# Kernel tuning notes

Hardware: AMD Instinct MI355X
Metric: run time of the kernel (lower is better)

The kernel has to match this reference:

```python
import jax, jax.numpy as jnp
import numpy as np
import math

B, L, H, NH = 8, 512, 512, 8
DH = H // NH


def setup_inputs() -> dict:
    key = jax.random.key(0)
    ks = jax.random.split(key, 12)
    src = jax.random.normal(ks[0], (B, L, H), dtype=jnp.float32)
    seq_len = jax.random.randint(ks[1], (B,), L // 2, L + 1).astype(jnp.int32)
    seq_len = seq_len.at[0].set(L)  # guarantee max(seq_len) == L
    pe = jax.random.normal(ks[2], (2 * L, H), dtype=jnp.float32) * 0.02
    s = 1.0 / math.sqrt(H)
    Wq = jax.random.normal(ks[3], (H, H), dtype=jnp.float32) * s
    bq = jnp.zeros((H,), jnp.float32)
    Wk = jax.random.normal(ks[4], (H, H), dtype=jnp.float32) * s
    bk = jnp.zeros((H,), jnp.float32)
    Wv = jax.random.normal(ks[5], (H, H), dtype=jnp.float32) * s
    bv = jnp.zeros((H,), jnp.float32)
    Wr = jax.random.normal(ks[6], (H, H), dtype=jnp.float32) * s
    br = jnp.zeros((H,), jnp.float32)
    u = jax.random.normal(ks[7], (NH, DH), dtype=jnp.float32) * 0.02
    v = jax.random.normal(ks[8], (NH, DH), dtype=jnp.float32) * 0.02
    gamma = jnp.ones((H,), jnp.float32)
    beta = jnp.zeros((H,), jnp.float32)
    return dict(src=src, seq_len=seq_len, pe=pe, Wq=Wq, bq=bq, Wk=Wk, bk=bk,
                Wv=Wv, bv=bv, Wr=Wr, br=br, u=u, v=v, gamma=gamma, beta=beta)


def reference(src, seq_len, pe, Wq, bq, Wk, bk, Wv, bv, Wr, br, u, v, gamma, beta):
    b, l, h = src.shape
    dh = h // NH
    # relative distance rel[i,j] = j - i, lookup pe[rel + L]  -> [L, L, H]
    rel = jnp.arange(l)[None, :] - jnp.arange(l)[:, None]
    R = pe[rel + l]
    # projections (torch Linear: y = x W^T + b)
    q = src @ Wq.T + bq
    k = src @ Wk.T + bk
    val = src @ Wv.T + bv
    R = R @ Wr.T + br
    # split heads
    q = q.reshape(b, l, NH, dh)
    k = k.reshape(b, l, NH, dh)
    val = val.reshape(b, l, NH, dh)
    R = R.reshape(l, l, NH, dh)
    # Transformer-XL score terms
    A = jnp.einsum('bihd,bjhd->bhij', q, k)
    Bt = jnp.einsum('bihd,ijhd->bhij', q, R)
    C = jnp.einsum('hd,bjhd->bhj', u, k)[:, :, None, :]
    D = jnp.einsum('ijhd,hd->hij', R, v)[None]
    scores = (A + Bt + C + D) / math.sqrt(dh)
    # key-side padding mask
    mask = jnp.arange(l)[None, :] < seq_len[:, None]  # [B, L]
    scores = jnp.where(mask[:, None, None, :], scores, jnp.float32(-1e15))
    attn = jax.nn.softmax(scores, axis=-1)
    out = jnp.einsum('bhij,bjhd->bihd', attn, val).reshape(b, l, h)
    res = src + out
    # LayerNorm (eps=1e-5) then exact GELU
    mu = jnp.mean(res, axis=-1, keepdims=True)
    var = jnp.mean((res - mu) ** 2, axis=-1, keepdims=True)
    ln = (res - mu) * jax.lax.rsqrt(var + 1e-5) * gamma + beta
    return jax.nn.gelu(ln, approximate=False)
```

## Files before the change

### kernel.cpp

```cpp
#include <hip/hip_runtime.h>
#include <math.h>

#define Bn 8
#define Ln 512
#define Hn 512
#define NHn 8
#define DHn 64

typedef __attribute__((ext_vector_type(8))) short short8;
typedef __attribute__((ext_vector_type(4))) float f32x4;

__device__ __forceinline__ unsigned short f2bf(float f) {
    unsigned int u = __float_as_uint(f);
    unsigned int r = (u + 0x7FFFu + ((u >> 16) & 1u)) >> 16;
    return (unsigned short)r;
}
__device__ __forceinline__ float bf2f(unsigned short s) {
    return __uint_as_float(((unsigned int)s) << 16);
}

__device__ __forceinline__ void gload_lds16(const void* g, void* l) {
    __builtin_amdgcn_global_load_lds(
        (const __attribute__((address_space(1))) unsigned int*)g,
        (__attribute__((address_space(3))) unsigned int*)l,
        16, 0, 0);
}

__global__ __launch_bounds__(256) void convert_kernel(
    const float* __restrict__ src, const float* __restrict__ pe,
    const float* __restrict__ Wq, const float* __restrict__ Wk,
    const float* __restrict__ Wv, const float* __restrict__ Wr,
    const float* __restrict__ bq, const float* __restrict__ bk,
    const float* __restrict__ bv,
    unsigned short* __restrict__ src_bf, unsigned short* __restrict__ pe_bf,
    unsigned short* __restrict__ Wcat_bf, unsigned short* __restrict__ Wr_bf,
    float* __restrict__ bcat)
{
    const int bid = blockIdx.x;
    const int tid = threadIdx.x;
    const float* in; unsigned short* outp; int base4;
    if (bid < 2048)      { in = src; outp = src_bf;           base4 = bid; }
    else if (bid < 2560) { in = pe;  outp = pe_bf;            base4 = bid - 2048; }
    else if (bid < 2816) { in = Wq;  outp = Wcat_bf;          base4 = bid - 2560; }
    else if (bid < 3072) { in = Wk;  outp = Wcat_bf + 262144; base4 = bid - 2816; }
    else if (bid < 3328) { in = Wv;  outp = Wcat_bf + 524288; base4 = bid - 3072; }
    else if (bid < 3584) { in = Wr;  outp = Wr_bf;            base4 = bid - 3328; }
    else {
        const int idx = (bid - 3584) * 256 + tid;
        if (idx < 512)            bcat[idx] = bq[idx];
        else if (idx < 1024)      bcat[idx] = bk[idx - 512];
        else if (idx < 1536)      bcat[idx] = bv[idx - 1024];
        return;
    }
    const int i4 = (base4 * 256 + tid) * 4;
    float4 x = *(const float4*)&in[i4];
    ushort4 o;
    o.x = f2bf(x.x); o.y = f2bf(x.y); o.z = f2bf(x.z); o.w = f2bf(x.w);
    *(ushort4*)&outp[i4] = o;
}

__global__ __launch_bounds__(256) void mfma_nt_kernel(
    const unsigned short* __restrict__ src_bf,
    const unsigned short* __restrict__ Wcat_bf,
    const float* __restrict__ bcat,
    unsigned short* __restrict__ QKb,
    unsigned short* __restrict__ VTg,
    const unsigned short* __restrict__ pe_bf,
    const unsigned short* __restrict__ Wr_bf,
    const float* __restrict__ br,
    unsigned short* __restrict__ Rpb)
{
    const unsigned short* A; const unsigned short* B;
    int m0, n0, mode;
    if (blockIdx.z == 0) {
        if (blockIdx.x < 8) {
            mode = 0; A = src_bf;  m0 = blockIdx.y * 128;
            B = Wcat_bf; n0 = blockIdx.x * 128;
        } else {
            mode = 1; A = Wcat_bf; m0 = blockIdx.x * 128;
            B = src_bf;  n0 = blockIdx.y * 128;
        }
    } else {
        if (blockIdx.x >= 4 || blockIdx.y >= 8) return;
        mode = 2; A = pe_bf; m0 = blockIdx.y * 128;
        B = Wr_bf; n0 = blockIdx.x * 128;
    }

    __shared__ unsigned short As[128 * 32];
    __shared__ unsigned short Bs[128 * 32];

    const int t = threadIdx.x;
    const int wave = t >> 6, lane = t & 63;
    const int wm = (wave >> 1) * 64;
    const int wn = (wave & 1) * 64;

    f32x4 acc[4][4] = {};

    const int srow = wave * 32 + (lane >> 2);
    const int scol = (lane & 3) * 8;
    const unsigned short* Ag = A + (size_t)(m0 + srow) * 512 + scol;
    const unsigned short* Bg = B + (size_t)(n0 + srow) * 512 + scol;
    unsigned short* AsW = &As[srow * 32 + scol];
    unsigned short* BsW = &Bs[srow * 32 + scol];

    for (int k0 = 0; k0 < 512; k0 += 32) {
        __syncthreads();
        gload_lds16(Ag + k0,            AsW);
        gload_lds16(Ag + k0 + 16 * 512, AsW + 16 * 32);
        gload_lds16(Bg + k0,            BsW);
        gload_lds16(Bg + k0 + 16 * 512, BsW + 16 * 32);
        __syncthreads();

        short8 af[4], bf[4];
        #pragma unroll
        for (int mt = 0; mt < 4; ++mt)
            af[mt] = *(const short8*)&As[(wm + mt * 16 + (lane & 15)) * 32 + (lane >> 4) * 8];
        #pragma unroll
        for (int nt = 0; nt < 4; ++nt)
            bf[nt] = *(const short8*)&Bs[(wn + nt * 16 + (lane & 15)) * 32 + (lane >> 4) * 8];
        #pragma unroll
        for (int mt = 0; mt < 4; ++mt)
            #pragma unroll
            for (int nt = 0; nt < 4; ++nt)
                acc[mt][nt] = __builtin_amdgcn_mfma_f32_16x16x32_bf16(
                    af[mt], bf[nt], acc[mt][nt], 0, 0, 0);
    }

    const int crow = (lane >> 4) * 4;
    const int ccol = lane & 15;
    if (mode == 0) {
        #pragma unroll
        for (int mt = 0; mt < 4; ++mt)
            #pragma unroll
            for (int nt = 0; nt < 4; ++nt) {
                const int n = n0 + wn + nt * 16 + ccol;
                const float bn = bcat[n];
                #pragma unroll
                for (int r = 0; r < 4; ++r) {
                    const int m = m0 + wm + mt * 16 + crow + r;
                    QKb[(size_t)m * 1024 + n] = f2bf(acc[mt][nt][r] + bn);
                }
            }
    } else if (mode == 1) {
        #pragma unroll
        for (int mt = 0; mt < 4; ++mt)
            #pragma unroll
            for (int nt = 0; nt < 4; ++nt) {
                const int n = n0 + wn + nt * 16 + ccol;
                #pragma unroll
                for (int r = 0; r < 4; ++r) {
                    const int m = m0 + wm + mt * 16 + crow + r;
                    VTg[(size_t)(m - 1024) * 4096 + n] = f2bf(acc[mt][nt][r] + bcat[m]);
                }
            }
    } else {
        #pragma unroll
        for (int mt = 0; mt < 4; ++mt)
            #pragma unroll
            for (int nt = 0; nt < 4; ++nt) {
                const int n = n0 + wn + nt * 16 + ccol;
                const float bn = br[n];
                #pragma unroll
                for (int r = 0; r < 4; ++r) {
                    const int m = m0 + wm + mt * 16 + crow + r;
                    Rpb[(size_t)m * 512 + n] = f2bf(acc[mt][nt][r] + bn);
                }
            }
    }
}

#define PADK 72
#define QRS 133
__global__ __launch_bounds__(256) void attn_kernel(
    const unsigned short* __restrict__ QKb,
    const unsigned short* __restrict__ VTg,
    const unsigned short* __restrict__ Rpb,
    const float* __restrict__ u, const float* __restrict__ v,
    const int* __restrict__ seq_len, float* __restrict__ O)
{
    const int i0 = blockIdx.x * 64;
    const int h  = blockIdx.y;
    const int b  = blockIdx.z;
    const int slen = seq_len[b];

    __shared__ unsigned short k_s [64 * PADK];
    __shared__ unsigned short vT_s[64 * PADK];
    __shared__ unsigned short rs_s[64 * PADK];
    __shared__ unsigned short p_s [64 * PADK];
    __shared__ unsigned short qrT [64 * QRS];

    const int t = threadIdx.x;
    const int wave = t >> 6, lane = t & 63;
    const int l = lane & 15, g = lane >> 4;

    short8 af_qu[2], af_qv[2];
    {
        const unsigned short* qrow =
            QKb + (size_t)(b * 512 + i0 + wave * 16 + l) * 1024 + h * 64;
        #pragma unroll
        for (int kk = 0; kk < 2; ++kk) {
            const int c = kk * 32 + g * 8;
            unsigned short q8[8];
            *(uint4*)q8 = *(const uint4*)(qrow + c);
            float4 u0 = *(const float4*)(u + h * 64 + c);
            float4 u1 = *(const float4*)(u + h * 64 + c + 4);
            float4 v0 = *(const float4*)(v + h * 64 + c);
            float4 v1 = *(const float4*)(v + h * 64 + c + 4);
            float uf[8] = {u0.x,u0.y,u0.z,u0.w,u1.x,u1.y,u1.z,u1.w};
            float vf[8] = {v0.x,v0.y,v0.z,v0.w,v1.x,v1.y,v1.z,v1.w};
            short8 qu, qv;
            #pragma unroll
            for (int e = 0; e < 8; ++e) {
                float qf = bf2f(q8[e]);
                qu[e] = (short)f2bf(qf + uf[e]);
                qv[e] = (short)f2bf(qf + vf[e]);
            }
            af_qu[kk] = qu; af_qv[kk] = qv;
        }
    }

    float m_run[4], l_run[4];
    f32x4 accO[4] = {};
    #pragma unroll
    for (int r = 0; r < 4; ++r) { m_run[r] = -3.0e38f; l_run[r] = 0.f; }

    const int jr = t >> 2, c0 = (t & 3) * 16;

    for (int jt = 0; jt < 8; ++jt) {
        const int j0 = jt * 64;
        __syncthreads();

        {
            const unsigned short* kp =
                QKb + (size_t)(b * 512 + j0 + jr) * 1024 + 512 + h * 64 + c0;
            *(uint4*)(k_s + jr * PADK + c0)     = *(const uint4*)(kp);
            *(uint4*)(k_s + jr * PADK + c0 + 8) = *(const uint4*)(kp + 8);
            const unsigned short* vp =
                VTg + (size_t)(h * 64 + jr) * 4096 + b * 512 + j0 + c0;
            *(uint4*)(vT_s + jr * PADK + c0)     = *(const uint4*)(vp);
            *(uint4*)(vT_s + jr * PADK + c0 + 8) = *(const uint4*)(vp + 8);
        }

        const int nchunk = (jt == 0) ? 2 : 1;
        for (int c = 0; c < nchunk; ++c) {
            const int g_base = (jt == 0) ? (448 - i0 + 64 * c) : (j0 - i0 + 512);
            {
                const unsigned short* rp =
                    Rpb + (size_t)(g_base + jr) * 512 + h * 64 + c0;
                *(uint4*)(rs_s + jr * PADK + c0)     = *(const uint4*)(rp);
                *(uint4*)(rs_s + jr * PADK + c0 + 8) = *(const uint4*)(rp + 8);
            }
            __syncthreads();
            const int slot0 = (g_base & 127);
            #pragma unroll
            for (int nt8 = 0; nt8 < 4; ++nt8) {
                f32x4 a = {};
                #pragma unroll
                for (int kk = 0; kk < 2; ++kk) {
                    short8 br8 = *(const short8*)&rs_s[(nt8 * 16 + l) * PADK + kk * 32 + g * 8];
                    a = __builtin_amdgcn_mfma_f32_16x16x32_bf16(af_qv[kk], br8, a, 0, 0, 0);
                }
                const int sl = slot0 + nt8 * 16 + l;
                #pragma unroll
                for (int r = 0; r < 4; ++r)
                    qrT[(wave * 16 + g * 4 + r) * QRS + sl] = f2bf(a[r]);
            }
            if (c + 1 < nchunk) __syncthreads();
        }
        __syncthreads();

        f32x4 accA[4];
        #pragma unroll
        for (int nt = 0; nt < 4; ++nt) {
            f32x4 a = {};
            #pragma unroll
            for (int kk = 0; kk < 2; ++kk) {
                short8 bk = *(const short8*)&k_s[(nt * 16 + l) * PADK + kk * 32 + g * 8];
                a = __builtin_amdgcn_mfma_f32_16x16x32_bf16(af_qu[kk], bk, a, 0, 0, 0);
            }
            accA[nt] = a;
        }

        float sv[4][4];
        #pragma unroll
        for (int nt = 0; nt < 4; ++nt)
            #pragma unroll
            for (int r = 0; r < 4; ++r) {
                const int il = wave * 16 + g * 4 + r;
                const int slot = (j0 + nt * 16 + l - i0 - il + 512) & 127;
                const float qr = bf2f(qrT[il * QRS + slot]);
                float s = (accA[nt][r] + qr) * 0.125f;
                if (j0 + nt * 16 + l >= slen) s = -1e15f;
                sv[nt][r] = s;
            }

        float alpha_r[4];
        #pragma unroll
        for (int r = 0; r < 4; ++r) {
            float tm = fmaxf(fmaxf(sv[0][r], sv[1][r]), fmaxf(sv[2][r], sv[3][r]));
            tm = fmaxf(tm, __shfl_xor(tm, 1, 64));
            tm = fmaxf(tm, __shfl_xor(tm, 2, 64));
            tm = fmaxf(tm, __shfl_xor(tm, 4, 64));
            tm = fmaxf(tm, __shfl_xor(tm, 8, 64));
            const float mn = fmaxf(m_run[r], tm);
            alpha_r[r] = __expf(m_run[r] - mn);
            m_run[r] = mn;
            float ss = 0.f;
            #pragma unroll
            for (int nt = 0; nt < 4; ++nt) {
                const float p = __expf(sv[nt][r] - mn);
                sv[nt][r] = p; ss += p;
            }
            ss += __shfl_xor(ss, 1, 64);
            ss += __shfl_xor(ss, 2, 64);
            ss += __shfl_xor(ss, 4, 64);
            ss += __shfl_xor(ss, 8, 64);
            l_run[r] = l_run[r] * alpha_r[r] + ss;
        }

        #pragma unroll
        for (int nt = 0; nt < 4; ++nt)
            #pragma unroll
            for (int r = 0; r < 4; ++r)
                p_s[(wave * 16 + g * 4 + r) * PADK + nt * 16 + l] = f2bf(sv[nt][r]);
        __builtin_amdgcn_sched_barrier(0);

        #pragma unroll
        for (int nt = 0; nt < 4; ++nt)
            #pragma unroll
            for (int r = 0; r < 4; ++r)
                accO[nt][r] *= alpha_r[r];

        short8 pa[2];
        #pragma unroll
        for (int kk = 0; kk < 2; ++kk)
            pa[kk] = *(const short8*)&p_s[(wave * 16 + l) * PADK + kk * 32 + g * 8];
        #pragma unroll
        for (int nt = 0; nt < 4; ++nt) {
            #pragma unroll
            for (int kk = 0; kk < 2; ++kk) {
                short8 bv8 = *(const short8*)&vT_s[(nt * 16 + l) * PADK + kk * 32 + g * 8];
                accO[nt] = __builtin_amdgcn_mfma_f32_16x16x32_bf16(pa[kk], bv8, accO[nt], 0, 0, 0);
            }
        }
    }

    float inv[4];
    #pragma unroll
    for (int r = 0; r < 4; ++r) inv[r] = 1.0f / l_run[r];
    #pragma unroll
    for (int nt = 0; nt < 4; ++nt)
        #pragma unroll
        for (int r = 0; r < 4; ++r)
            O[(size_t)(b * 512 + i0 + wave * 16 + g * 4 + r) * 512 + h * 64 + nt * 16 + l]
                = accO[nt][r] * inv[r];
}

__global__ __launch_bounds__(256) void ln_gelu_kernel(
    const float* __restrict__ src, const float* __restrict__ O,
    const float* __restrict__ gamma, const float* __restrict__ beta,
    float* __restrict__ out)
{
    const int row  = blockIdx.x * 4 + (threadIdx.x >> 6);
    const int lane = threadIdx.x & 63;
    const float* s = &src[(size_t)row * 512];
    const float* o = &O[(size_t)row * 512];
    float x[8];
    float sum = 0.f;
    #pragma unroll
    for (int e = 0; e < 8; ++e) {
        x[e] = s[lane + e * 64] + o[lane + e * 64];
        sum += x[e];
    }
    #pragma unroll
    for (int off = 32; off >= 1; off >>= 1) sum += __shfl_xor(sum, off, 64);
    const float mean = sum * (1.0f / 512.0f);
    float var = 0.f;
    #pragma unroll
    for (int e = 0; e < 8; ++e) { float d = x[e] - mean; var += d * d; }
    #pragma unroll
    for (int off = 32; off >= 1; off >>= 1) var += __shfl_xor(var, off, 64);
    var *= (1.0f / 512.0f);
    const float inv = rsqrtf(var + 1e-5f);
    #pragma unroll
    for (int e = 0; e < 8; ++e) {
        const int c = lane + e * 64;
        float ln = (x[e] - mean) * inv * gamma[c] + beta[c];
        out[(size_t)row * 512 + c] = 0.5f * ln * (1.0f + erff(ln * 0.70710678118654752f));
    }
}

extern "C" void kernel_launch(void* const* d_in, const int* in_sizes, int n_in,
                              void* d_out, int out_size, void* d_ws, size_t ws_size,
                              hipStream_t stream)
{
    const float* src     = (const float*)d_in[0];
    const int*   seq_len = (const int*)  d_in[1];
    const float* pe      = (const float*)d_in[2];
    const float* Wq      = (const float*)d_in[3];
    const float* bq      = (const float*)d_in[4];
    const float* Wk      = (const float*)d_in[5];
    const float* bk      = (const float*)d_in[6];
    const float* Wv      = (const float*)d_in[7];
    const float* bv      = (const float*)d_in[8];
    const float* Wr      = (const float*)d_in[9];
    const float* br      = (const float*)d_in[10];
    const float* u       = (const float*)d_in[11];
    const float* v       = (const float*)d_in[12];
    const float* gamma   = (const float*)d_in[13];
    const float* beta    = (const float*)d_in[14];
    float* out = (float*)d_out;

    char* w = (char*)d_ws;
    unsigned short* QKb     = (unsigned short*)(w);
    unsigned short* VTg     = (unsigned short*)(w + 8388608);
    unsigned short* Rpb     = (unsigned short*)(w + 12582912);
    float*          O       = (float*)         (w + 13631488);
    unsigned short* src_bf  = (unsigned short*)(w + 22020096);
    unsigned short* pe_bf   = (unsigned short*)(w + 26214400);
    unsigned short* Wcat_bf = (unsigned short*)(w + 27262976);
    unsigned short* Wr_bf   = (unsigned short*)(w + 28835840);
    float*          bcat    = (float*)         (w + 29360128);

    convert_kernel<<<dim3(3590), 256, 0, stream>>>(
        src, pe, Wq, Wk, Wv, Wr, bq, bk, bv,
        src_bf, pe_bf, Wcat_bf, Wr_bf, bcat);

    mfma_nt_kernel<<<dim3(12, 32, 2), 256, 0, stream>>>(
        src_bf, Wcat_bf, bcat, QKb, VTg,
        pe_bf, Wr_bf, br, Rpb);

    attn_kernel<<<dim3(8, NHn, Bn), 256, 0, stream>>>(QKb, VTg, Rpb, u, v, seq_len, O);

    ln_gelu_kernel<<<dim3(Bn * Ln / 4), 256, 0, stream>>>(src, O, gamma, beta, out);
}
```

Baseline: 142.1 us.

## Prefetch attention tiles into registers, compact GEMM grid, bf16 attention output

The attention kernel now loads the next K, V and R tiles into registers while it computes the current tile. It also hoists the extra first R chunk out of the loop, which removes one barrier per iteration. The GEMM launch changes from a padded 3D grid with many early-exiting blocks to a dense 1D grid of 416 blocks. The attention output is written as bf16 instead of fp32, and LayerNorm uses vectorized loads and stores. The bf16 output adds rounding error before the residual add, and the register prefetch raises register pressure.

```diff
diff --git a/kernel.cpp b/kernel.cpp
--- a/kernel.cpp
+++ b/kernel.cpp
@@ -59,31 +59,31 @@
     *(ushort4*)&outp[i4] = o;
 }
 
-__global__ __launch_bounds__(256) void mfma_nt_kernel(
+__global__ __launch_bounds__(256) void gemm_kernel(
     const unsigned short* __restrict__ src_bf,
     const unsigned short* __restrict__ Wcat_bf,
-    const float* __restrict__ bcat,
+    const unsigned short* __restrict__ pe_bf,
+    const unsigned short* __restrict__ Wr_bf,
+    const float* __restrict__ bcat, const float* __restrict__ br,
     unsigned short* __restrict__ QKb,
     unsigned short* __restrict__ VTg,
-    const unsigned short* __restrict__ pe_bf,
-    const unsigned short* __restrict__ Wr_bf,
-    const float* __restrict__ br,
     unsigned short* __restrict__ Rpb)
 {
-    const unsigned short* A; const unsigned short* B;
-    int m0, n0, mode;
-    if (blockIdx.z == 0) {
-        if (blockIdx.x < 8) {
-            mode = 0; A = src_bf;  m0 = blockIdx.y * 128;
-            B = Wcat_bf; n0 = blockIdx.x * 128;
-        } else {
-            mode = 1; A = Wcat_bf; m0 = blockIdx.x * 128;
-            B = src_bf;  n0 = blockIdx.y * 128;
-        }
+    const int bid = blockIdx.x;
+    int mode, m0, n0;
+    const unsigned short *A, *B;
+    if (bid < 256) {
+        mode = 0; n0 = (bid & 7) * 128; m0 = (bid >> 3) * 128;
+        A = src_bf + (size_t)m0 * 512;
+        B = Wcat_bf + (size_t)n0 * 512;
+    } else if (bid < 384) {
+        mode = 1; m0 = ((bid - 256) & 3) * 128; n0 = ((bid - 256) >> 2) * 128;
+        A = Wcat_bf + (size_t)(1024 + m0) * 512;
+        B = src_bf + (size_t)n0 * 512;
     } else {
-        if (blockIdx.x >= 4 || blockIdx.y >= 8) return;
-        mode = 2; A = pe_bf; m0 = blockIdx.y * 128;
-        B = Wr_bf; n0 = blockIdx.x * 128;
+        mode = 2; n0 = ((bid - 384) & 3) * 128; m0 = ((bid - 384) >> 2) * 128;
+        A = pe_bf + (size_t)m0 * 512;
+        B = Wr_bf + (size_t)n0 * 512;
     }
 
     __shared__ unsigned short As[128 * 32];
@@ -98,8 +98,8 @@
 
     const int srow = wave * 32 + (lane >> 2);
     const int scol = (lane & 3) * 8;
-    const unsigned short* Ag = A + (size_t)(m0 + srow) * 512 + scol;
-    const unsigned short* Bg = B + (size_t)(n0 + srow) * 512 + scol;
+    const unsigned short* Ag = A + (size_t)srow * 512 + scol;
+    const unsigned short* Bg = B + (size_t)srow * 512 + scol;
     unsigned short* AsW = &As[srow * 32 + scol];
     unsigned short* BsW = &Bs[srow * 32 + scol];
 
@@ -149,8 +149,8 @@
                 const int n = n0 + wn + nt * 16 + ccol;
                 #pragma unroll
                 for (int r = 0; r < 4; ++r) {
-                    const int m = m0 + wm + mt * 16 + crow + r;
-                    VTg[(size_t)(m - 1024) * 4096 + n] = f2bf(acc[mt][nt][r] + bcat[m]);
+                    const int dv = m0 + wm + mt * 16 + crow + r;
+                    VTg[(size_t)dv * 4096 + n] = f2bf(acc[mt][nt][r] + bcat[1024 + dv]);
                 }
             }
     } else {
@@ -176,7 +176,7 @@
     const unsigned short* __restrict__ VTg,
     const unsigned short* __restrict__ Rpb,
     const float* __restrict__ u, const float* __restrict__ v,
-    const int* __restrict__ seq_len, float* __restrict__ O)
+    const int* __restrict__ seq_len, unsigned short* __restrict__ Ob)
 {
     const int i0 = blockIdx.x * 64;
     const int h  = blockIdx.y;
@@ -226,48 +226,62 @@
 
     const int jr = t >> 2, c0 = (t & 3) * 16;
 
+    auto btChunk = [&](int slot0) {
+        #pragma unroll
+        for (int nt8 = 0; nt8 < 4; ++nt8) {
+            f32x4 a = {};
+            #pragma unroll
+            for (int kk = 0; kk < 2; ++kk) {
+                short8 br8 = *(const short8*)&rs_s[(nt8 * 16 + l) * PADK + kk * 32 + g * 8];
+                a = __builtin_amdgcn_mfma_f32_16x16x32_bf16(af_qv[kk], br8, a, 0, 0, 0);
+            }
+            const int sl = slot0 + nt8 * 16 + l;
+            #pragma unroll
+            for (int r = 0; r < 4; ++r)
+                qrT[(wave * 16 + g * 4 + r) * QRS + sl] = f2bf(a[r]);
+        }
+    };
+
+    const unsigned short* rpA = Rpb + (size_t)(448 - i0 + jr) * 512 + h * 64 + c0;
+    uint4 rA0 = *(const uint4*)(rpA);
+    uint4 rA1 = *(const uint4*)(rpA + 8);
+    const unsigned short* kp0 = QKb + (size_t)(b * 512 + jr) * 1024 + 512 + h * 64 + c0;
+    uint4 kc0 = *(const uint4*)(kp0), kc1 = *(const uint4*)(kp0 + 8);
+    const unsigned short* vp0 = VTg + (size_t)(h * 64 + jr) * 4096 + b * 512 + c0;
+    uint4 vc0 = *(const uint4*)(vp0), vc1 = *(const uint4*)(vp0 + 8);
+    const unsigned short* rp0 = Rpb + (size_t)(512 - i0 + jr) * 512 + h * 64 + c0;
+    uint4 rc0 = *(const uint4*)(rp0), rc1 = *(const uint4*)(rp0 + 8);
+
+    *(uint4*)(rs_s + jr * PADK + c0)     = rA0;
+    *(uint4*)(rs_s + jr * PADK + c0 + 8) = rA1;
+    __syncthreads();
+    btChunk((448 - i0) & 127);
+
     for (int jt = 0; jt < 8; ++jt) {
         const int j0 = jt * 64;
         __syncthreads();
 
-        {
+        *(uint4*)(k_s  + jr * PADK + c0)     = kc0;
+        *(uint4*)(k_s  + jr * PADK + c0 + 8) = kc1;
+        *(uint4*)(vT_s + jr * PADK + c0)     = vc0;
+        *(uint4*)(vT_s + jr * PADK + c0 + 8) = vc1;
+        *(uint4*)(rs_s + jr * PADK + c0)     = rc0;
+        *(uint4*)(rs_s + jr * PADK + c0 + 8) = rc1;
+        __syncthreads();
+
+        if (jt < 7) {
             const unsigned short* kp =
-                QKb + (size_t)(b * 512 + j0 + jr) * 1024 + 512 + h * 64 + c0;
-            *(uint4*)(k_s + jr * PADK + c0)     = *(const uint4*)(kp);
-            *(uint4*)(k_s + jr * PADK + c0 + 8) = *(const uint4*)(kp + 8);
+                QKb + (size_t)(b * 512 + j0 + 64 + jr) * 1024 + 512 + h * 64 + c0;
+            kc0 = *(const uint4*)(kp); kc1 = *(const uint4*)(kp + 8);
             const unsigned short* vp =
-                VTg + (size_t)(h * 64 + jr) * 4096 + b * 512 + j0 + c0;
-            *(uint4*)(vT_s + jr * PADK + c0)     = *(const uint4*)(vp);
-            *(uint4*)(vT_s + jr * PADK + c0 + 8) = *(const uint4*)(vp + 8);
-        }
-
-        const int nchunk = (jt == 0) ? 2 : 1;
-        for (int c = 0; c < nchunk; ++c) {
-            const int g_base = (jt == 0) ? (448 - i0 + 64 * c) : (j0 - i0 + 512);
-            {
-                const unsigned short* rp =
-                    Rpb + (size_t)(g_base + jr) * 512 + h * 64 + c0;
-                *(uint4*)(rs_s + jr * PADK + c0)     = *(const uint4*)(rp);
-                *(uint4*)(rs_s + jr * PADK + c0 + 8) = *(const uint4*)(rp + 8);
-            }
-            __syncthreads();
-            const int slot0 = (g_base & 127);
-            #pragma unroll
-            for (int nt8 = 0; nt8 < 4; ++nt8) {
-                f32x4 a = {};
-                #pragma unroll
-                for (int kk = 0; kk < 2; ++kk) {
-                    short8 br8 = *(const short8*)&rs_s[(nt8 * 16 + l) * PADK + kk * 32 + g * 8];
-                    a = __builtin_amdgcn_mfma_f32_16x16x32_bf16(af_qv[kk], br8, a, 0, 0, 0);
-                }
-                const int sl = slot0 + nt8 * 16 + l;
-                #pragma unroll
-                for (int r = 0; r < 4; ++r)
-                    qrT[(wave * 16 + g * 4 + r) * QRS + sl] = f2bf(a[r]);
-            }
-            if (c + 1 < nchunk) __syncthreads();
-        }
-        __syncthreads();
+                VTg + (size_t)(h * 64 + jr) * 4096 + b * 512 + j0 + 64 + c0;
+            vc0 = *(const uint4*)(vp); vc1 = *(const uint4*)(vp + 8);
+            const unsigned short* rp =
+                Rpb + (size_t)(j0 + 64 - i0 + 512 + jr) * 512 + h * 64 + c0;
+            rc0 = *(const uint4*)(rp); rc1 = *(const uint4*)(rp + 8);
+        }
+
+        btChunk((j0 - i0 + 512) & 127);
 
         f32x4 accA[4];
         #pragma unroll
@@ -275,8 +289,8 @@
             f32x4 a = {};
             #pragma unroll
             for (int kk = 0; kk < 2; ++kk) {
-                short8 bk = *(const short8*)&k_s[(nt * 16 + l) * PADK + kk * 32 + g * 8];
-                a = __builtin_amdgcn_mfma_f32_16x16x32_bf16(af_qu[kk], bk, a, 0, 0, 0);
+                short8 bk8 = *(const short8*)&k_s[(nt * 16 + l) * PADK + kk * 32 + g * 8];
+                a = __builtin_amdgcn_mfma_f32_16x16x32_bf16(af_qu[kk], bk8, a, 0, 0, 0);
             }
             accA[nt] = a;
         }
@@ -308,8 +322,8 @@
             float ss = 0.f;
             #pragma unroll
             for (int nt = 0; nt < 4; ++nt) {
-                const float p = __expf(sv[nt][r] - mn);
-                sv[nt][r] = p; ss += p;
+                const float pe_ = __expf(sv[nt][r] - mn);
+                sv[nt][r] = pe_; ss += pe_;
             }
             ss += __shfl_xor(ss, 1, 64);
             ss += __shfl_xor(ss, 2, 64);
@@ -323,7 +337,6 @@
             #pragma unroll
             for (int r = 0; r < 4; ++r)
                 p_s[(wave * 16 + g * 4 + r) * PADK + nt * 16 + l] = f2bf(sv[nt][r]);
-        __builtin_amdgcn_sched_barrier(0);
 
         #pragma unroll
         for (int nt = 0; nt < 4; ++nt)
@@ -352,26 +365,31 @@
     for (int nt = 0; nt < 4; ++nt)
         #pragma unroll
         for (int r = 0; r < 4; ++r)
-            O[(size_t)(b * 512 + i0 + wave * 16 + g * 4 + r) * 512 + h * 64 + nt * 16 + l]
-                = accO[nt][r] * inv[r];
+            Ob[(size_t)(b * 512 + i0 + wave * 16 + g * 4 + r) * 512 + h * 64 + nt * 16 + l]
+                = f2bf(accO[nt][r] * inv[r]);
 }
 
 __global__ __launch_bounds__(256) void ln_gelu_kernel(
-    const float* __restrict__ src, const float* __restrict__ O,
+    const float* __restrict__ src, const unsigned short* __restrict__ Ob,
     const float* __restrict__ gamma, const float* __restrict__ beta,
     float* __restrict__ out)
 {
     const int row  = blockIdx.x * 4 + (threadIdx.x >> 6);
     const int lane = threadIdx.x & 63;
-    const float* s = &src[(size_t)row * 512];
-    const float* o = &O[(size_t)row * 512];
+    const int c0   = lane * 8;
+    const float* s = &src[(size_t)row * 512 + c0];
+    float4 s0 = *(const float4*)(s);
+    float4 s1 = *(const float4*)(s + 4);
+    unsigned short o8[8];
+    *(uint4*)o8 = *(const uint4*)(Ob + (size_t)row * 512 + c0);
     float x[8];
+    x[0] = s0.x + bf2f(o8[0]); x[1] = s0.y + bf2f(o8[1]);
+    x[2] = s0.z + bf2f(o8[2]); x[3] = s0.w + bf2f(o8[3]);
+    x[4] = s1.x + bf2f(o8[4]); x[5] = s1.y + bf2f(o8[5]);
+    x[6] = s1.z + bf2f(o8[6]); x[7] = s1.w + bf2f(o8[7]);
     float sum = 0.f;
     #pragma unroll
-    for (int e = 0; e < 8; ++e) {
-        x[e] = s[lane + e * 64] + o[lane + e * 64];
-        sum += x[e];
-    }
+    for (int e = 0; e < 8; ++e) sum += x[e];
     #pragma unroll
     for (int off = 32; off >= 1; off >>= 1) sum += __shfl_xor(sum, off, 64);
     const float mean = sum * (1.0f / 512.0f);
@@ -382,12 +400,21 @@
     for (int off = 32; off >= 1; off >>= 1) var += __shfl_xor(var, off, 64);
     var *= (1.0f / 512.0f);
     const float inv = rsqrtf(var + 1e-5f);
+    float4 g0 = *(const float4*)(gamma + c0);
+    float4 g1 = *(const float4*)(gamma + c0 + 4);
+    float4 b0 = *(const float4*)(beta + c0);
+    float4 b1 = *(const float4*)(beta + c0 + 4);
+    float gm[8] = {g0.x,g0.y,g0.z,g0.w,g1.x,g1.y,g1.z,g1.w};
+    float bt[8] = {b0.x,b0.y,b0.z,b0.w,b1.x,b1.y,b1.z,b1.w};
+    float r8[8];
     #pragma unroll
     for (int e = 0; e < 8; ++e) {
-        const int c = lane + e * 64;
-        float ln = (x[e] - mean) * inv * gamma[c] + beta[c];
-        out[(size_t)row * 512 + c] = 0.5f * ln * (1.0f + erff(ln * 0.70710678118654752f));
-    }
+        float ln = (x[e] - mean) * inv * gm[e] + bt[e];
+        r8[e] = 0.5f * ln * (1.0f + erff(ln * 0.70710678118654752f));
+    }
+    float* op = &out[(size_t)row * 512 + c0];
+    *(float4*)(op)     = make_float4(r8[0], r8[1], r8[2], r8[3]);
+    *(float4*)(op + 4) = make_float4(r8[4], r8[5], r8[6], r8[7]);
 }
 
 extern "C" void kernel_launch(void* const* d_in, const int* in_sizes, int n_in,
@@ -415,22 +442,21 @@
     unsigned short* QKb     = (unsigned short*)(w);
     unsigned short* VTg     = (unsigned short*)(w + 8388608);
     unsigned short* Rpb     = (unsigned short*)(w + 12582912);
-    float*          O       = (float*)         (w + 13631488);
-    unsigned short* src_bf  = (unsigned short*)(w + 22020096);
-    unsigned short* pe_bf   = (unsigned short*)(w + 26214400);
-    unsigned short* Wcat_bf = (unsigned short*)(w + 27262976);
-    unsigned short* Wr_bf   = (unsigned short*)(w + 28835840);
-    float*          bcat    = (float*)         (w + 29360128);
+    unsigned short* Ob      = (unsigned short*)(w + 13631488);
+    unsigned short* src_bf  = (unsigned short*)(w + 17825792);
+    unsigned short* pe_bf   = (unsigned short*)(w + 22020096);
+    unsigned short* Wcat_bf = (unsigned short*)(w + 23068672);
+    unsigned short* Wr_bf   = (unsigned short*)(w + 24641536);
+    float*          bcat    = (float*)         (w + 25165824);
 
     convert_kernel<<<dim3(3590), 256, 0, stream>>>(
         src, pe, Wq, Wk, Wv, Wr, bq, bk, bv,
         src_bf, pe_bf, Wcat_bf, Wr_bf, bcat);
 
-    mfma_nt_kernel<<<dim3(12, 32, 2), 256, 0, stream>>>(
-        src_bf, Wcat_bf, bcat, QKb, VTg,
-        pe_bf, Wr_bf, br, Rpb);
-
-    attn_kernel<<<dim3(8, NHn, Bn), 256, 0, stream>>>(QKb, VTg, Rpb, u, v, seq_len, O);
-
-    ln_gelu_kernel<<<dim3(Bn * Ln / 4), 256, 0, stream>>>(src, O, gamma, beta, out);
-}
+    gemm_kernel<<<dim3(416), 256, 0, stream>>>(
+        src_bf, Wcat_bf, pe_bf, Wr_bf, bcat, br, QKb, VTg, Rpb);
+
+    attn_kernel<<<dim3(8, NHn, Bn), 256, 0, stream>>>(QKb, VTg, Rpb, u, v, seq_len, Ob);
+
+    ln_gelu_kernel<<<dim3(Bn * Ln / 4), 256, 0, stream>>>(src, Ob, gamma, beta, out);
+}
```

Result: faster. 137.6 us (-3.2%).
